# Kernel optimization log

Hardware: AMD Instinct MI355X
Metric: run time of the kernel (lower is better)

The kernel has to match this reference:

```python
import jax, jax.numpy as jnp
import numpy as np

H = 16  # num_heads (matches init_kwargs)


def setup_inputs() -> dict:
    key = jax.random.key(0)
    ks = jax.random.split(key, 5)
    B, T, C = 4, 2048, 2048
    S = C // H
    g = 0.5 * (6.0 / (C + C)) ** 0.5 * (3.0 ** 0.5)  # ~xavier_uniform scale, gain 0.5
    x = jax.random.normal(ks[0], (B, T, C), dtype=jnp.float32)
    Wk = jax.random.uniform(ks[1], (C, C), jnp.float32, -g, g)
    Wv = jax.random.uniform(ks[2], (C, C), jnp.float32, -g, g)
    Wr = jax.random.uniform(ks[3], (C, C), jnp.float32, -g, g)
    Wo = jax.random.uniform(ks[4], (C, C), jnp.float32, -g, g)
    time_decay = jnp.full((H, S), -5.0, dtype=jnp.float32)
    time_first = jnp.zeros((H, S), dtype=jnp.float32)
    return {"x": x, "Wk": Wk, "Wv": Wv, "Wr": Wr, "Wo": Wo,
            "time_decay": time_decay, "time_first": time_first}


def _wkv(k, v, time_decay, time_first):
    # k, v: [B, T, H, S] float32
    decay = jnp.exp(-jnp.exp(time_decay.astype(jnp.float32)))  # [H, S]
    first = jnp.exp(time_first.astype(jnp.float32))            # [H, S]
    w = jnp.exp(jnp.clip(k.astype(jnp.float32), -10.0, 10.0))  # [B, T, H, S]
    # t==0 branch (state = first*w0*v0) == uniform recurrence with w0 scaled by first
    w = w.at[:, 0].multiply(first)
    wt = jnp.swapaxes(w, 0, 1)                    # [T, B, H, S]
    vt = jnp.swapaxes(v.astype(jnp.float32), 0, 1)

    def step(carry, inp):
        num, den = carry
        w_t, v_t = inp
        num = decay * num + w_t * v_t
        den = decay * den + w_t
        return (num, den), num / (den + 1e-6)

    B, _, _, S = k.shape
    init = (jnp.zeros((B, H, S), jnp.float32), jnp.zeros((B, H, S), jnp.float32))
    _, wkv = jax.lax.scan(step, init, (wt, vt))   # [T, B, H, S]
    return jnp.swapaxes(wkv, 0, 1).astype(k.dtype)  # [B, T, H, S]


def reference(x, Wk, Wv, Wr, Wo, time_decay, time_first):
    B, T, C = x.shape
    S = C // H
    k = (x @ Wk.T).reshape(B, T, H, S)
    v = (x @ Wv.T).reshape(B, T, H, S)
    r = (x @ Wr.T).reshape(B, T, H, S)
    wkv = _wkv(k, v, time_decay, time_first)
    rwkv = (jax.nn.sigmoid(r) * wkv).reshape(B, T, C)
    return rwkv @ Wo.T
```

## Files before the change

### kernel.cpp

```cpp
#include <hip/hip_runtime.h>
#include <hip/hip_bf16.h>

using bf16 = __hip_bfloat16;
using floatx4 = __attribute__((ext_vector_type(4))) float;
using bf16x8  = __attribute__((ext_vector_type(8))) __bf16;

#define MDIM 8192
#define NDIM 2048
#define KDIM 2048
#define TSEQ 2048
#define BB   4
#define CDIM 2048
#define NCHUNK 16
#define TCHUNK 128

typedef __attribute__((address_space(1))) void gvoid_t;
typedef __attribute__((address_space(3))) void lvoid_t;

__device__ __forceinline__ void load_lds16(const void* g, void* l) {
  __builtin_amdgcn_global_load_lds((gvoid_t*)(void*)g, (lvoid_t*)l, 16, 0, 0);
}

__global__ __launch_bounds__(256) void cvt_f32_bf16(const float* __restrict__ s,
                                                    __bf16* __restrict__ d, int n) {
  int i = (blockIdx.x * 256 + threadIdx.x) * 8;
  const int stride = gridDim.x * 256 * 8;
  for (; i < n; i += stride) {
    float4 a = *(const float4*)(s + i);
    float4 b = *(const float4*)(s + i + 4);
    bf16x8 o;
    o[0] = (__bf16)a.x; o[1] = (__bf16)a.y; o[2] = (__bf16)a.z; o[3] = (__bf16)a.w;
    o[4] = (__bf16)b.x; o[5] = (__bf16)b.y; o[6] = (__bf16)b.z; o[7] = (__bf16)b.w;
    *(bf16x8*)(d + i) = o;
  }
}

template <typename CT>
__device__ __forceinline__ void gemm_body(const __bf16* __restrict__ A,
                                          const __bf16* __restrict__ B,
                                          CT* __restrict__ C) {
  __shared__ __bf16 sA[128 * 32];
  __shared__ __bf16 sB[128 * 32];
  const int tid  = threadIdx.x;
  const int lane = tid & 63;
  const int wave = tid >> 6;
  const int wm = (wave >> 1) * 64;
  const int wn = (wave & 1) * 64;
  const int bm = blockIdx.x, bn = blockIdx.y;

  floatx4 acc[4][4] = {};

  const int arow = tid >> 2;
  const int acol = (tid & 3) * 8;
  const __bf16* Ag = A + (size_t)(bm * 128 + arow) * KDIM + acol;
  const __bf16* Bg = B + (size_t)(bn * 128 + arow) * KDIM + acol;
  __bf16* sAp = sA + tid * 8;
  __bf16* sBp = sB + tid * 8;
  const int fr = lane & 15;
  const int fk = (lane >> 4) * 8;

  for (int kt = 0; kt < KDIM; kt += 32) {
    load_lds16(Ag,                      sAp);
    load_lds16(Ag + (size_t)64 * KDIM,  sAp + 64 * 32);
    load_lds16(Bg,                      sBp);
    load_lds16(Bg + (size_t)64 * KDIM,  sBp + 64 * 32);
    Ag += 32; Bg += 32;
    __syncthreads();

    bf16x8 af[4], bfr[4];
#pragma unroll
    for (int i = 0; i < 4; ++i)
      af[i] = *(const bf16x8*)(sA + (wm + i * 16 + fr) * 32 + fk);
#pragma unroll
    for (int j = 0; j < 4; ++j)
      bfr[j] = *(const bf16x8*)(sB + (wn + j * 16 + fr) * 32 + fk);
#pragma unroll
    for (int i = 0; i < 4; ++i)
#pragma unroll
      for (int j = 0; j < 4; ++j)
        acc[i][j] = __builtin_amdgcn_mfma_f32_16x16x32_bf16(af[i], bfr[j], acc[i][j], 0, 0, 0);
    __syncthreads();
  }

  const int crow = (lane >> 4) * 4;
  const int ccol = lane & 15;
#pragma unroll
  for (int i = 0; i < 4; ++i)
#pragma unroll
    for (int j = 0; j < 4; ++j) {
      const size_t r0 = (size_t)(bm * 128 + wm + i * 16 + crow);
      const int    c0 = bn * 128 + wn + j * 16 + ccol;
#pragma unroll
      for (int rg = 0; rg < 4; ++rg)
        C[(r0 + rg) * NDIM + c0] = (CT)(acc[i][j][rg]);
    }
}

__global__ __launch_bounds__(256) void gemm_qkv(const __bf16* __restrict__ x,
                                                const __bf16* __restrict__ Wk,
                                                const __bf16* __restrict__ Wv,
                                                const __bf16* __restrict__ Wr,
                                                __bf16* __restrict__ kb,
                                                __bf16* __restrict__ vb,
                                                __bf16* __restrict__ rb) {
  const __bf16* Bsel = (blockIdx.z == 0) ? Wk : (blockIdx.z == 1) ? Wv : Wr;
  __bf16*       Csel = (blockIdx.z == 0) ? kb : (blockIdx.z == 1) ? vb : rb;
  gemm_body<__bf16>(x, Bsel, Csel);
}

__global__ __launch_bounds__(256) void gemm_o(const __bf16* __restrict__ A,
                                              const __bf16* __restrict__ B,
                                              float* __restrict__ C) {
  gemm_body<float>(A, B, C);
}

__global__ __launch_bounds__(256) void wkv_summary(
    const __bf16* __restrict__ kb, const __bf16* __restrict__ vb,
    const float* __restrict__ td, const float* __restrict__ tf,
    float* __restrict__ nsum, float* __restrict__ dsum) {
  const int c = blockIdx.x * 256 + threadIdx.x;
  const int chunk = blockIdx.y;
  const int b = blockIdx.z;
  const float ed = __expf(td[c]);
  const float decay = __expf(-ed);
  const float first = __expf(tf[c]);
  size_t base = ((size_t)b * TSEQ + (size_t)chunk * TCHUNK) * CDIM + c;
  float num = 0.f, den = 0.f;
#pragma unroll 4
  for (int t = 0; t < TCHUNK; ++t) {
    float kk = (float)kb[base + (size_t)t * CDIM];
    float vv = (float)vb[base + (size_t)t * CDIM];
    kk = fminf(fmaxf(kk, -10.f), 10.f);
    float w = __expf(kk);
    if (chunk == 0 && t == 0) w *= first;
    num = decay * num + w * vv;
    den = decay * den + w;
  }
  const int si = (chunk * BB + b) * CDIM + c;
  nsum[si] = num;
  dsum[si] = den;
}

__global__ __launch_bounds__(256) void wkv_apply(
    const __bf16* __restrict__ kb, const __bf16* __restrict__ vb,
    __bf16* __restrict__ rb,
    const float* __restrict__ td, const float* __restrict__ tf,
    const float* __restrict__ nsum, const float* __restrict__ dsum) {
  const int c = blockIdx.x * 256 + threadIdx.x;
  const int chunk = blockIdx.y;
  const int b = blockIdx.z;
  const float ed = __expf(td[c]);
  const float decay = __expf(-ed);
  const float dTC = __expf(-ed * (float)TCHUNK);
  const float first = __expf(tf[c]);

  float num = 0.f, den = 0.f;
  for (int j = 0; j < chunk; ++j) {
    const int si = (j * BB + b) * CDIM + c;
    num = dTC * num + nsum[si];
    den = dTC * den + dsum[si];
  }
  size_t base = ((size_t)b * TSEQ + (size_t)chunk * TCHUNK) * CDIM + c;
#pragma unroll 2
  for (int t = 0; t < TCHUNK; ++t) {
    const size_t idx = base + (size_t)t * CDIM;
    float kk = (float)kb[idx];
    float vv = (float)vb[idx];
    kk = fminf(fmaxf(kk, -10.f), 10.f);
    float w = __expf(kk);
    if (chunk == 0 && t == 0) w *= first;
    num = decay * num + w * vv;
    den = decay * den + w;
    const float wkv = num / (den + 1e-6f);
    const float r = (float)rb[idx];
    const float sr = 1.f / (1.f + __expf(-r));
    rb[idx] = (__bf16)(sr * wkv);
  }
}

extern "C" void kernel_launch(void* const* d_in, const int* in_sizes, int n_in,
                              void* d_out, int out_size, void* d_ws, size_t ws_size,
                              hipStream_t stream) {
  const float* x  = (const float*)d_in[0];
  const float* Wk = (const float*)d_in[1];
  const float* Wv = (const float*)d_in[2];
  const float* Wr = (const float*)d_in[3];
  const float* Wo = (const float*)d_in[4];
  const float* td = (const float*)d_in[5];
  const float* tf = (const float*)d_in[6];
  float* out = (float*)d_out;

  char* ws = (char*)d_ws;
  const size_t matX = (size_t)MDIM * KDIM * sizeof(__bf16);
  const size_t matW = (size_t)NDIM * KDIM * sizeof(__bf16);
  __bf16* xb  = (__bf16*)(ws);
  __bf16* wkb = (__bf16*)(ws + matX);
  __bf16* wvb = (__bf16*)(ws + matX + matW);
  __bf16* wrb = (__bf16*)(ws + matX + 2 * matW);
  __bf16* wob = (__bf16*)(ws + matX + 3 * matW);
  __bf16* kb  = (__bf16*)(ws + matX + 4 * matW);
  __bf16* vb  = (__bf16*)(ws + 2 * matX + 4 * matW);
  __bf16* rb  = (__bf16*)(ws + 3 * matX + 4 * matW);
  float* nsum = (float*)(ws + 4 * matX + 4 * matW);
  float* dsum = nsum + NCHUNK * BB * CDIM;

  dim3 blk(256);
  const int nx = MDIM * KDIM, nw = NDIM * KDIM;
  cvt_f32_bf16<<<dim3(nx / (8 * 256)), blk, 0, stream>>>(x,  xb,  nx);
  cvt_f32_bf16<<<dim3(nw / (8 * 256)), blk, 0, stream>>>(Wk, wkb, nw);
  cvt_f32_bf16<<<dim3(nw / (8 * 256)), blk, 0, stream>>>(Wv, wvb, nw);
  cvt_f32_bf16<<<dim3(nw / (8 * 256)), blk, 0, stream>>>(Wr, wrb, nw);
  cvt_f32_bf16<<<dim3(nw / (8 * 256)), blk, 0, stream>>>(Wo, wob, nw);

  dim3 gq(MDIM / 128, NDIM / 128, 3);
  gemm_qkv<<<gq, blk, 0, stream>>>(xb, wkb, wvb, wrb, kb, vb, rb);
  dim3 gw(CDIM / 256, NCHUNK, BB);
  wkv_summary<<<gw, blk, 0, stream>>>(kb, vb, td, tf, nsum, dsum);
  wkv_apply<<<gw, blk, 0, stream>>>(kb, vb, rb, td, tf, nsum, dsum);
  dim3 go(MDIM / 128, NDIM / 128, 1);
  gemm_o<<<go, blk, 0, stream>>>(rb, wob, out);
}
```

Measured before the change: 556.8 us.

## Vectorize WKV scan to two channels per thread, halve chunk size, merge weight converts

The WKV summary and apply kernels now handle two adjacent channels per thread, using bf16x2 loads and stores and float2 chunk summaries. The chunk length drops from 128 to 64 steps, giving 32 chunks, which keeps the grid the same size while shortening each serial scan. Division and the sigmoid reciprocal now use the fast rcp instruction. The four weight conversion launches are merged into one. The wider accesses and shorter serial chain aim to cut memory transactions, per-thread latency and launch overhead, at the cost of a longer prefix loop over chunk summaries in wkv_apply and slightly lower precision from rcp.

```diff
diff --git a/kernel.cpp b/kernel.cpp
--- a/kernel.cpp
+++ b/kernel.cpp
@@ -4,6 +4,7 @@
 using bf16 = __hip_bfloat16;
 using floatx4 = __attribute__((ext_vector_type(4))) float;
 using bf16x8  = __attribute__((ext_vector_type(8))) __bf16;
+using bf16x2  = __attribute__((ext_vector_type(2))) __bf16;
 
 #define MDIM 8192
 #define NDIM 2048
@@ -11,8 +12,8 @@
 #define TSEQ 2048
 #define BB   4
 #define CDIM 2048
-#define NCHUNK 16
-#define TCHUNK 128
+#define NCHUNK 32
+#define TCHUNK 64
 
 typedef __attribute__((address_space(1))) void gvoid_t;
 typedef __attribute__((address_space(3))) void lvoid_t;
@@ -21,18 +22,36 @@
   __builtin_amdgcn_global_load_lds((gvoid_t*)(void*)g, (lvoid_t*)l, 16, 0, 0);
 }
 
-__global__ __launch_bounds__(256) void cvt_f32_bf16(const float* __restrict__ s,
-                                                    __bf16* __restrict__ d, int n) {
-  int i = (blockIdx.x * 256 + threadIdx.x) * 8;
-  const int stride = gridDim.x * 256 * 8;
-  for (; i < n; i += stride) {
-    float4 a = *(const float4*)(s + i);
-    float4 b = *(const float4*)(s + i + 4);
-    bf16x8 o;
-    o[0] = (__bf16)a.x; o[1] = (__bf16)a.y; o[2] = (__bf16)a.z; o[3] = (__bf16)a.w;
-    o[4] = (__bf16)b.x; o[5] = (__bf16)b.y; o[6] = (__bf16)b.z; o[7] = (__bf16)b.w;
-    *(bf16x8*)(d + i) = o;
-  }
+__global__ __launch_bounds__(256) void cvt_x(const float* __restrict__ s,
+                                             __bf16* __restrict__ d) {
+  const int i = (blockIdx.x * 256 + threadIdx.x) * 8;
+  float4 a = *(const float4*)(s + i);
+  float4 b = *(const float4*)(s + i + 4);
+  bf16x8 o;
+  o[0] = (__bf16)a.x; o[1] = (__bf16)a.y; o[2] = (__bf16)a.z; o[3] = (__bf16)a.w;
+  o[4] = (__bf16)b.x; o[5] = (__bf16)b.y; o[6] = (__bf16)b.z; o[7] = (__bf16)b.w;
+  *(bf16x8*)(d + i) = o;
+}
+
+__global__ __launch_bounds__(256) void cvt_w(const float* __restrict__ s0,
+                                             const float* __restrict__ s1,
+                                             const float* __restrict__ s2,
+                                             const float* __restrict__ s3,
+                                             __bf16* __restrict__ d0,
+                                             __bf16* __restrict__ d1,
+                                             __bf16* __restrict__ d2,
+                                             __bf16* __restrict__ d3) {
+  const float* s = (blockIdx.y == 0) ? s0 : (blockIdx.y == 1) ? s1
+                 : (blockIdx.y == 2) ? s2 : s3;
+  __bf16*      d = (blockIdx.y == 0) ? d0 : (blockIdx.y == 1) ? d1
+                 : (blockIdx.y == 2) ? d2 : d3;
+  const int i = (blockIdx.x * 256 + threadIdx.x) * 8;
+  float4 a = *(const float4*)(s + i);
+  float4 b = *(const float4*)(s + i + 4);
+  bf16x8 o;
+  o[0] = (__bf16)a.x; o[1] = (__bf16)a.y; o[2] = (__bf16)a.z; o[3] = (__bf16)a.w;
+  o[4] = (__bf16)b.x; o[5] = (__bf16)b.y; o[6] = (__bf16)b.z; o[7] = (__bf16)b.w;
+  *(bf16x8*)(d + i) = o;
 }
 
 template <typename CT>
@@ -118,27 +137,31 @@
     const __bf16* __restrict__ kb, const __bf16* __restrict__ vb,
     const float* __restrict__ td, const float* __restrict__ tf,
     float* __restrict__ nsum, float* __restrict__ dsum) {
-  const int c = blockIdx.x * 256 + threadIdx.x;
+  const int c0 = (blockIdx.x * 256 + threadIdx.x) * 2;
   const int chunk = blockIdx.y;
   const int b = blockIdx.z;
-  const float ed = __expf(td[c]);
-  const float decay = __expf(-ed);
-  const float first = __expf(tf[c]);
-  size_t base = ((size_t)b * TSEQ + (size_t)chunk * TCHUNK) * CDIM + c;
-  float num = 0.f, den = 0.f;
+  const float dc0 = __expf(-__expf(td[c0]));
+  const float dc1 = __expf(-__expf(td[c0 + 1]));
+  const float fi0 = __expf(tf[c0]);
+  const float fi1 = __expf(tf[c0 + 1]);
+  size_t base = ((size_t)b * TSEQ + (size_t)chunk * TCHUNK) * CDIM + c0;
+  float n0 = 0.f, d0 = 0.f, n1 = 0.f, d1 = 0.f;
 #pragma unroll 4
   for (int t = 0; t < TCHUNK; ++t) {
-    float kk = (float)kb[base + (size_t)t * CDIM];
-    float vv = (float)vb[base + (size_t)t * CDIM];
-    kk = fminf(fmaxf(kk, -10.f), 10.f);
-    float w = __expf(kk);
-    if (chunk == 0 && t == 0) w *= first;
-    num = decay * num + w * vv;
-    den = decay * den + w;
-  }
-  const int si = (chunk * BB + b) * CDIM + c;
-  nsum[si] = num;
-  dsum[si] = den;
+    bf16x2 k2 = *(const bf16x2*)(kb + base + (size_t)t * CDIM);
+    bf16x2 v2 = *(const bf16x2*)(vb + base + (size_t)t * CDIM);
+    float k0f = fminf(fmaxf((float)k2[0], -10.f), 10.f);
+    float k1f = fminf(fmaxf((float)k2[1], -10.f), 10.f);
+    float w0 = __expf(k0f), w1 = __expf(k1f);
+    if (chunk == 0 && t == 0) { w0 *= fi0; w1 *= fi1; }
+    n0 = dc0 * n0 + w0 * (float)v2[0];
+    d0 = dc0 * d0 + w0;
+    n1 = dc1 * n1 + w1 * (float)v2[1];
+    d1 = dc1 * d1 + w1;
+  }
+  const size_t si = (size_t)(chunk * BB + b) * CDIM + c0;
+  *(float2*)(nsum + si) = make_float2(n0, n1);
+  *(float2*)(dsum + si) = make_float2(d0, d1);
 }
 
 __global__ __launch_bounds__(256) void wkv_apply(
@@ -146,35 +169,49 @@
     __bf16* __restrict__ rb,
     const float* __restrict__ td, const float* __restrict__ tf,
     const float* __restrict__ nsum, const float* __restrict__ dsum) {
-  const int c = blockIdx.x * 256 + threadIdx.x;
+  const int c0 = (blockIdx.x * 256 + threadIdx.x) * 2;
   const int chunk = blockIdx.y;
   const int b = blockIdx.z;
-  const float ed = __expf(td[c]);
-  const float decay = __expf(-ed);
-  const float dTC = __expf(-ed * (float)TCHUNK);
-  const float first = __expf(tf[c]);
-
-  float num = 0.f, den = 0.f;
+  const float ed0 = __expf(td[c0]);
+  const float ed1 = __expf(td[c0 + 1]);
+  const float dc0 = __expf(-ed0);
+  const float dc1 = __expf(-ed1);
+  const float dT0 = __expf(-ed0 * (float)TCHUNK);
+  const float dT1 = __expf(-ed1 * (float)TCHUNK);
+  const float fi0 = __expf(tf[c0]);
+  const float fi1 = __expf(tf[c0 + 1]);
+
+  float n0 = 0.f, d0 = 0.f, n1 = 0.f, d1 = 0.f;
   for (int j = 0; j < chunk; ++j) {
-    const int si = (j * BB + b) * CDIM + c;
-    num = dTC * num + nsum[si];
-    den = dTC * den + dsum[si];
-  }
-  size_t base = ((size_t)b * TSEQ + (size_t)chunk * TCHUNK) * CDIM + c;
+    const size_t si = (size_t)(j * BB + b) * CDIM + c0;
+    float2 ns = *(const float2*)(nsum + si);
+    float2 ds = *(const float2*)(dsum + si);
+    n0 = dT0 * n0 + ns.x;  d0 = dT0 * d0 + ds.x;
+    n1 = dT1 * n1 + ns.y;  d1 = dT1 * d1 + ds.y;
+  }
+  size_t base = ((size_t)b * TSEQ + (size_t)chunk * TCHUNK) * CDIM + c0;
 #pragma unroll 2
   for (int t = 0; t < TCHUNK; ++t) {
     const size_t idx = base + (size_t)t * CDIM;
-    float kk = (float)kb[idx];
-    float vv = (float)vb[idx];
-    kk = fminf(fmaxf(kk, -10.f), 10.f);
-    float w = __expf(kk);
-    if (chunk == 0 && t == 0) w *= first;
-    num = decay * num + w * vv;
-    den = decay * den + w;
-    const float wkv = num / (den + 1e-6f);
-    const float r = (float)rb[idx];
-    const float sr = 1.f / (1.f + __expf(-r));
-    rb[idx] = (__bf16)(sr * wkv);
+    bf16x2 k2 = *(const bf16x2*)(kb + idx);
+    bf16x2 v2 = *(const bf16x2*)(vb + idx);
+    bf16x2 r2 = *(const bf16x2*)(rb + idx);
+    float k0f = fminf(fmaxf((float)k2[0], -10.f), 10.f);
+    float k1f = fminf(fmaxf((float)k2[1], -10.f), 10.f);
+    float w0 = __expf(k0f), w1 = __expf(k1f);
+    if (chunk == 0 && t == 0) { w0 *= fi0; w1 *= fi1; }
+    n0 = dc0 * n0 + w0 * (float)v2[0];
+    d0 = dc0 * d0 + w0;
+    n1 = dc1 * n1 + w1 * (float)v2[1];
+    d1 = dc1 * d1 + w1;
+    const float wkv0 = n0 * __builtin_amdgcn_rcpf(d0 + 1e-6f);
+    const float wkv1 = n1 * __builtin_amdgcn_rcpf(d1 + 1e-6f);
+    const float sr0 = __builtin_amdgcn_rcpf(1.f + __expf(-(float)r2[0]));
+    const float sr1 = __builtin_amdgcn_rcpf(1.f + __expf(-(float)r2[1]));
+    bf16x2 o;
+    o[0] = (__bf16)(sr0 * wkv0);
+    o[1] = (__bf16)(sr1 * wkv1);
+    *(bf16x2*)(rb + idx) = o;
   }
 }
 
@@ -202,19 +239,16 @@
   __bf16* vb  = (__bf16*)(ws + 2 * matX + 4 * matW);
   __bf16* rb  = (__bf16*)(ws + 3 * matX + 4 * matW);
   float* nsum = (float*)(ws + 4 * matX + 4 * matW);
-  float* dsum = nsum + NCHUNK * BB * CDIM;
+  float* dsum = nsum + (size_t)NCHUNK * BB * CDIM;
 
   dim3 blk(256);
-  const int nx = MDIM * KDIM, nw = NDIM * KDIM;
-  cvt_f32_bf16<<<dim3(nx / (8 * 256)), blk, 0, stream>>>(x,  xb,  nx);
-  cvt_f32_bf16<<<dim3(nw / (8 * 256)), blk, 0, stream>>>(Wk, wkb, nw);
-  cvt_f32_bf16<<<dim3(nw / (8 * 256)), blk, 0, stream>>>(Wv, wvb, nw);
-  cvt_f32_bf16<<<dim3(nw / (8 * 256)), blk, 0, stream>>>(Wr, wrb, nw);
-  cvt_f32_bf16<<<dim3(nw / (8 * 256)), blk, 0, stream>>>(Wo, wob, nw);
+  cvt_x<<<dim3(MDIM * KDIM / (8 * 256)), blk, 0, stream>>>(x, xb);
+  cvt_w<<<dim3(NDIM * KDIM / (8 * 256), 4), blk, 0, stream>>>(
+      Wk, Wv, Wr, Wo, wkb, wvb, wrb, wob);
 
   dim3 gq(MDIM / 128, NDIM / 128, 3);
   gemm_qkv<<<gq, blk, 0, stream>>>(xb, wkb, wvb, wrb, kb, vb, rb);
-  dim3 gw(CDIM / 256, NCHUNK, BB);
+  dim3 gw(CDIM / 512, NCHUNK, BB);
   wkv_summary<<<gw, blk, 0, stream>>>(kb, vb, td, tf, nsum, dsum);
   wkv_apply<<<gw, blk, 0, stream>>>(kb, vb, rb, td, tf, nsum, dsum);
   dim3 go(MDIM / 128, NDIM / 128, 1);
```

Result: faster. 539.1 us (-3.2%).
